# Optimization experiments

Measured on AMD Instinct MI355X. Metric: run time of the kernel, lower is better.

## Reference

```python
import jax, jax.numpy as jnp
import numpy as np

B, S, H, D = 2, 2048, 16, 64


def setup_inputs() -> dict:
    key0 = jax.random.key(0)
    kq, kk = jax.random.split(key0)
    query = jax.random.normal(kq, (B, S, H, D), dtype=jnp.float32)
    key = jax.random.normal(kk, (B, S, H, D), dtype=jnp.float32)
    # causal mask, broadcastable to [B, H, q, k]
    mask = jnp.tril(jnp.ones((S, S), dtype=bool))[None, None, :, :]
    mask = jnp.broadcast_to(mask, (B, 1, S, S))
    return {"query": query, "key": key, "mask": mask}


def reference(query, key, mask):
    dtype = query.dtype
    qk_features = query.shape[-1]
    q = query / jnp.sqrt(qk_features).astype(dtype)
    # [B, H, q, k]
    attn_weights = jnp.einsum('...qhd,...khd->...hqk', q, key)
    big_neg = jnp.finfo(dtype).min
    attn_weights = jnp.where(mask, attn_weights, big_neg)
    attn_weights = jax.nn.softmax(attn_weights).astype(dtype)
    return attn_weights
```

## Files before the change

### kernel.cpp

```cpp
#include <hip/hip_runtime.h>
#include <stdint.h>
#include <stddef.h>

#define B_ 2
#define H_ 16
#define S_ 2048
#define D_ 64

#define TQ 32
#define TK 256
#define NW 4
#define BLK (NW*64)
#define NQT (S_/TQ)
#define NBLK_F (B_*H_*NQT)
#define NBLK_S (32*36)
#define NBLK_W (32*8*4)

typedef __attribute__((ext_vector_type(8))) short bf16x8;
typedef __attribute__((ext_vector_type(4))) float f32x4;

__device__ __forceinline__ unsigned short f2bf(float f) {
  union { float f; uint32_t u; } v; v.f = f;
  uint32_t r = v.u + 0x7FFFu + ((v.u >> 16) & 1u);
  return (unsigned short)(r >> 16);
}

__device__ __forceinline__ void stage_k(const f32x4* kp, unsigned short* ldsK,
                                        int b, int h, int kc, int tid) {
#pragma unroll
  for (int i = 0; i < 8; ++i) {
    const int g  = i * BLK + tid;
    const int kl = g >> 3;
    const int gd = g & 7;
    const size_t gb = (((size_t)b * S_ + (kc * TK + kl)) * H_ + h) * (D_ / 4) + gd * 2;
    f32x4 v0 = kp[gb];
    f32x4 v1 = kp[gb + 1];
    bf16x8 bv;
    bv[0] = (short)f2bf(v0.x); bv[1] = (short)f2bf(v0.y);
    bv[2] = (short)f2bf(v0.z); bv[3] = (short)f2bf(v0.w);
    bv[4] = (short)f2bf(v1.x); bv[5] = (short)f2bf(v1.y);
    bv[6] = (short)f2bf(v1.z); bv[7] = (short)f2bf(v1.w);
    const int idx = (kl * D_ + gd * 8) ^ ((kl & 7) << 3);
    *reinterpret_cast<bf16x8*>(&ldsK[idx]) = bv;
  }
}

__device__ __forceinline__ void stage_q(const f32x4* qp, unsigned short (*ldsQ)[72],
                                        int b, int h, int qb, int tid) {
#pragma unroll
  for (int i = 0; i < 2; ++i) {
    const int g   = i * BLK + tid;
    const int row = g >> 4;
    const int d4  = g & 15;
    f32x4 v = qp[(((size_t)b * S_ + (qb + row)) * H_ + h) * (D_ / 4) + d4];
    unsigned short* dst = &ldsQ[row][d4 * 4];
    dst[0] = f2bf(v.x * 0.125f);
    dst[1] = f2bf(v.y * 0.125f);
    dst[2] = f2bf(v.z * 0.125f);
    dst[3] = f2bf(v.w * 0.125f);
  }
}

struct QPre { f32x4 a, b; };
__device__ __forceinline__ QPre qpre_load(const f32x4* qp, int b, int h, int qb, int tid) {
  QPre r;
  {
    const int g = tid;
    r.a = qp[(((size_t)b * S_ + (qb + (g >> 4))) * H_ + h) * (D_ / 4) + (g & 15)];
  }
  {
    const int g = BLK + tid;
    r.b = qp[(((size_t)b * S_ + (qb + (g >> 4))) * H_ + h) * (D_ / 4) + (g & 15)];
  }
  return r;
}
__device__ __forceinline__ void qpre_write(unsigned short (*ldsQ)[72], const QPre& p, int tid) {
#pragma unroll
  for (int i = 0; i < 2; ++i) {
    const int g   = i * BLK + tid;
    const int row = g >> 4;
    const int d4  = g & 15;
    const f32x4 v = i ? p.b : p.a;
    unsigned short* dst = &ldsQ[row][d4 * 4];
    dst[0] = f2bf(v.x * 0.125f);
    dst[1] = f2bf(v.y * 0.125f);
    dst[2] = f2bf(v.z * 0.125f);
    dst[3] = f2bf(v.w * 0.125f);
  }
}

__device__ __forceinline__ void load_qfr(const unsigned short (*ldsQ)[72],
                                         bf16x8 qfr[2][2], int colk, int rg) {
#pragma unroll
  for (int qf = 0; qf < 2; ++qf)
#pragma unroll
    for (int hh = 0; hh < 2; ++hh)
      qfr[qf][hh] = *reinterpret_cast<const bf16x8*>(&ldsQ[qf * 16 + colk][hh * 32 + rg * 8]);
}

__device__ __forceinline__ void mfma_tile(const unsigned short* ldsK,
                                          const bf16x8 qfr[2][2],
                                          f32x4 acc[4][2], int w, int colk, int rg) {
#pragma unroll
  for (int kf = 0; kf < 4; ++kf) {
    const int krow = w * 64 + kf * 16 + colk;
    const int i0 = (krow * D_ + rg * 8) ^ ((krow & 7) << 3);
    const int i1 = (krow * D_ + 32 + rg * 8) ^ ((krow & 7) << 3);
    bf16x8 a0 = *reinterpret_cast<const bf16x8*>(&ldsK[i0]);
    bf16x8 a1 = *reinterpret_cast<const bf16x8*>(&ldsK[i1]);
#pragma unroll
    for (int qf = 0; qf < 2; ++qf) {
      acc[kf][qf] = __builtin_amdgcn_mfma_f32_16x16x32_bf16(a0, qfr[qf][0], acc[kf][qf], 0, 0, 0);
      acc[kf][qf] = __builtin_amdgcn_mfma_f32_16x16x32_bf16(a1, qfr[qf][1], acc[kf][qf], 0, 0, 0);
    }
  }
}

__global__ __launch_bounds__(BLK, 4)
void attn_sums_v4(const float* __restrict__ Qg, const float* __restrict__ Kg,
                  float* __restrict__ wsPart) {
  __shared__ unsigned short ldsK[TK * D_];
  __shared__ unsigned short ldsQ[TQ][72];
  __shared__ float ldsSum[NW][2][16];

  const int tid  = threadIdx.x;
  const int lane = tid & 63;
  const int w    = tid >> 6;
  const int colk = lane & 15;
  const int rg   = lane >> 4;

  int bid = (int)blockIdx.x;
  bid = (bid & 7) * (NBLK_S / 8) + (bid >> 3);
  const int bh = bid / 36;
  int j = bid - bh * 36;
  int kc = 0, base = 0;
  while (j >= base + (8 - kc)) { base += 8 - kc; ++kc; }
  const int ci = j - base;
  const int qt0 = kc * 8 + ci * 8;
  const int b = bh >> 4, h = bh & (H_ - 1);

  const f32x4* qp = reinterpret_cast<const f32x4*>(Qg);
  const f32x4* kp = reinterpret_cast<const f32x4*>(Kg);

  stage_k(kp, ldsK, b, h, kc, tid);

  for (int i = 0; i < 8; ++i) {
    const int qt = qt0 + i;
    const int qb = qt * TQ;
    __syncthreads();
    stage_q(qp, ldsQ, b, h, qb, tid);
    __syncthreads();
    bf16x8 qfr[2][2];
    load_qfr(ldsQ, qfr, colk, rg);
    f32x4 acc[4][2];
#pragma unroll
    for (int kf = 0; kf < 4; ++kf)
#pragma unroll
      for (int qf = 0; qf < 2; ++qf) acc[kf][qf] = (f32x4)0.0f;
    mfma_tile(ldsK, qfr, acc, w, colk, rg);

    float rsum[2] = {0.f, 0.f};
#pragma unroll
    for (int kf = 0; kf < 4; ++kf)
#pragma unroll
      for (int qf = 0; qf < 2; ++qf)
#pragma unroll
        for (int r = 0; r < 4; ++r) {
          const int kk = kc * TK + w * 64 + kf * 16 + rg * 4 + r;
          const int qq = qb + qf * 16 + colk;
          rsum[qf] += (kk <= qq) ? __expf(acc[kf][qf][r]) : 0.f;
        }
#pragma unroll
    for (int qf = 0; qf < 2; ++qf) {
      float v = rsum[qf];
      v += __shfl_xor(v, 16);
      v += __shfl_xor(v, 32);
      rsum[qf] = v;
    }
    if (rg == 0) { ldsSum[w][0][colk] = rsum[0]; ldsSum[w][1][colk] = rsum[1]; }
    __syncthreads();
    if (tid < 32) {
      const int qf = tid >> 4, ck = tid & 15;
      const float s = ldsSum[0][qf][ck] + ldsSum[1][qf][ck] +
                      ldsSum[2][qf][ck] + ldsSum[3][qf][ck];
      wsPart[((size_t)bh * 8 + kc) * S_ + qb + tid] = s;
    }
  }
}

__global__ __launch_bounds__(BLK, 4)
void attn_store_v6(const float* __restrict__ Qg, const float* __restrict__ Kg,
                   const float* __restrict__ wsPart, float* __restrict__ Og) {
  __shared__ unsigned short ldsK[TK * D_];
  __shared__ unsigned short ldsQ[TQ][72];
  __shared__ float rinvL[512];

  const int tid  = threadIdx.x;
  const int lane = tid & 63;
  const int w    = tid >> 6;
  const int colk = lane & 15;
  const int rg   = lane >> 4;

  int bid = (int)blockIdx.x;
  bid = (bid & 7) * (NBLK_W / 8) + (bid >> 3);
  const int bh = bid >> 5;
  const int r5 = bid & 31;
  const int kc = r5 >> 2;
  const int qg = r5 & 3;
  const int b = bh >> 4, h = bh & (H_ - 1);
  const int kmin = kc * TK;
  const int row0 = qg * 512;

  if (kmin > row0 + 511) {
    f32x4 z = {0.f, 0.f, 0.f, 0.f};
#pragma unroll 4
    for (int it = 0; it < 128; ++it) {
      const int g = it * BLK + tid;
      const int row = row0 + (g >> 6);
      const int cg = g & 63;
      __builtin_nontemporal_store(z, reinterpret_cast<f32x4*>(
          Og + ((size_t)bh * S_ + row) * S_ + kmin + cg * 4));
    }
    return;
  }

  const f32x4* qp = reinterpret_cast<const f32x4*>(Qg);
  const f32x4* kp = reinterpret_cast<const f32x4*>(Kg);

  const int i0 = (kmin > row0) ? ((kmin - row0) >> 5) : 0;

  if (i0 > 0) {
    f32x4 z = {0.f, 0.f, 0.f, 0.f};
#pragma unroll 4
    for (int it = 0; it < 64; ++it) {
      const int g = it * BLK + tid;
      const int row = row0 + (g >> 6);
      const int cg = g & 63;
      __builtin_nontemporal_store(z, reinterpret_cast<f32x4*>(
          Og + ((size_t)bh * S_ + row) * S_ + kmin + cg * 4));
    }
  }

  stage_k(kp, ldsK, b, h, kc, tid);

  for (int lr = tid; lr < 512; lr += BLK) {
    const int q = row0 + lr;
    if (q >= kmin) {
      float s = 0.f;
      const int top = q >> 8;
      for (int c2 = 0; c2 <= top; ++c2)
        s += wsPart[((size_t)bh * 8 + c2) * S_ + q];
      rinvL[lr] = 1.0f / s;
    }
  }

  stage_q(qp, ldsQ, b, h, row0 + i0 * TQ, tid);
  __syncthreads();

  QPre pre;
  if (i0 + 1 < 16) pre = qpre_load(qp, b, h, row0 + (i0 + 1) * TQ, tid);

  for (int i = i0; i < 16; ++i) {
    const int qb = row0 + i * TQ;
    float* outT = Og + ((size_t)bh * S_ + qb) * S_ + kmin;

    bf16x8 qfr[2][2];
    load_qfr(ldsQ, qfr, colk, rg);
    asm volatile("s_waitcnt lgkmcnt(0)" ::: "memory");
    __builtin_amdgcn_sched_barrier(0);
    __builtin_amdgcn_s_barrier();

    if (i + 1 < 16) {
      qpre_write(ldsQ, pre, tid);
      if (i + 2 < 16) pre = qpre_load(qp, b, h, row0 + (i + 2) * TQ, tid);
      asm volatile("s_waitcnt lgkmcnt(0)" ::: "memory");
    }
    __builtin_amdgcn_s_barrier();

    f32x4 acc[4][2];
#pragma unroll
    for (int kf = 0; kf < 4; ++kf)
#pragma unroll
      for (int qf = 0; qf < 2; ++qf) acc[kf][qf] = (f32x4)0.0f;
    mfma_tile(ldsK, qfr, acc, w, colk, rg);

#pragma unroll
    for (int kf = 0; kf < 4; ++kf)
#pragma unroll
      for (int qf = 0; qf < 2; ++qf) {
        const int qq = qb + qf * 16 + colk;
        const float ri = rinvL[i * 32 + qf * 16 + colk];
        f32x4 o;
#pragma unroll
        for (int r = 0; r < 4; ++r) {
          const int kk = kmin + w * 64 + kf * 16 + rg * 4 + r;
          o[r] = (kk <= qq) ? __expf(acc[kf][qf][r]) * ri : 0.f;
        }
        __builtin_nontemporal_store(o, reinterpret_cast<f32x4*>(
            outT + (size_t)(qf * 16 + colk) * S_ + w * 64 + kf * 16 + rg * 4));
      }
  }
}

__global__ __launch_bounds__(BLK, 4)
void attn_weights_fused(const float* __restrict__ Qg, const float* __restrict__ Kg,
                        float* __restrict__ Og) {
  __shared__ unsigned short ldsK[TK * D_];
  __shared__ unsigned short ldsQ[TQ][72];
  __shared__ float ldsSum[NW][2][16];

  const int tid  = threadIdx.x;
  const int lane = tid & 63;
  const int w    = tid >> 6;
  const int colk = lane & 15;
  const int rg   = lane >> 4;

  int bid = (int)blockIdx.x;
  bid = (bid & 7) * (NBLK_F / 8) + (bid >> 3);
  const int qt = bid & (NQT - 1);
  const int bh = bid >> 6;
  const int h  = bh & (H_ - 1);
  const int b  = bh >> 4;
  const int qb = qt * TQ;
  const int tmax = qb >> 8;

  float* outp = Og + ((size_t)bh * S_ + qb) * S_;
  {
    const int row = tid >> 3;
    f32x4 z = {0.f, 0.f, 0.f, 0.f};
    float* rp = outp + (size_t)row * S_;
    for (int c = (tmax + 1) * (TK / 4) + (tid & 7); c < S_ / 4; c += 8)
      *reinterpret_cast<f32x4*>(rp + c * 4) = z;
  }
  const f32x4* qp = reinterpret_cast<const f32x4*>(Qg);
  const f32x4* kp = reinterpret_cast<const f32x4*>(Kg);
  stage_q(qp, ldsQ, b, h, qb, tid);
  __syncthreads();
  bf16x8 qfr[2][2];
  load_qfr(ldsQ, qfr, colk, rg);
  float rsum[2] = {0.f, 0.f};
  for (int t = 0; t <= tmax; ++t) {
    stage_k(kp, ldsK, b, h, t, tid);
    __syncthreads();
    f32x4 acc[4][2];
#pragma unroll
    for (int kf = 0; kf < 4; ++kf)
#pragma unroll
      for (int qf = 0; qf < 2; ++qf) acc[kf][qf] = (f32x4)0.0f;
    mfma_tile(ldsK, qfr, acc, w, colk, rg);
#pragma unroll
    for (int kf = 0; kf < 4; ++kf)
#pragma unroll
      for (int qf = 0; qf < 2; ++qf)
#pragma unroll
        for (int r = 0; r < 4; ++r) {
          const int kk = t * TK + w * 64 + kf * 16 + rg * 4 + r;
          const int qq = qb + qf * 16 + colk;
          rsum[qf] += (kk <= qq) ? __expf(acc[kf][qf][r]) : 0.f;
        }
    __syncthreads();
  }
#pragma unroll
  for (int qf = 0; qf < 2; ++qf) {
    float v = rsum[qf];
    v += __shfl_xor(v, 16);
    v += __shfl_xor(v, 32);
    rsum[qf] = v;
  }
  if (rg == 0) { ldsSum[w][0][colk] = rsum[0]; ldsSum[w][1][colk] = rsum[1]; }
  __syncthreads();
  float rinv[2];
#pragma unroll
  for (int qf = 0; qf < 2; ++qf)
    rinv[qf] = 1.0f / (ldsSum[0][qf][colk] + ldsSum[1][qf][colk] +
                       ldsSum[2][qf][colk] + ldsSum[3][qf][colk]);
  for (int t = 0; t <= tmax; ++t) {
    stage_k(kp, ldsK, b, h, t, tid);
    __syncthreads();
    f32x4 acc[4][2];
#pragma unroll
    for (int kf = 0; kf < 4; ++kf)
#pragma unroll
      for (int qf = 0; qf < 2; ++qf) acc[kf][qf] = (f32x4)0.0f;
    mfma_tile(ldsK, qfr, acc, w, colk, rg);
#pragma unroll
    for (int kf = 0; kf < 4; ++kf)
#pragma unroll
      for (int qf = 0; qf < 2; ++qf) {
        f32x4 o;
#pragma unroll
        for (int r = 0; r < 4; ++r) {
          const int kk = t * TK + w * 64 + kf * 16 + rg * 4 + r;
          const int qq = qb + qf * 16 + colk;
          o[r] = (kk <= qq) ? __expf(acc[kf][qf][r]) * rinv[qf] : 0.f;
        }
        *reinterpret_cast<f32x4*>(outp + (size_t)(qf * 16 + colk) * S_ +
                                  t * TK + w * 64 + kf * 16 + rg * 4) = o;
      }
    __syncthreads();
  }
}

extern "C" void kernel_launch(void* const* d_in, const int* in_sizes, int n_in,
                              void* d_out, int out_size, void* d_ws, size_t ws_size,
                              hipStream_t stream) {
  const float* Qg = (const float*)d_in[0];
  const float* Kg = (const float*)d_in[1];
  float* Og = (float*)d_out;
  const size_t need = (size_t)32 * 8 * S_ * sizeof(float);
  if (ws_size >= need) {
    float* wsPart = (float*)d_ws;
    attn_sums_v4 <<<dim3(NBLK_S), dim3(BLK), 0, stream>>>(Qg, Kg, wsPart);
    attn_store_v6<<<dim3(NBLK_W), dim3(BLK), 0, stream>>>(Qg, Kg, wsPart, Og);
  } else {
    attn_weights_fused<<<dim3(NBLK_F), dim3(BLK), 0, stream>>>(Qg, Kg, Og);
  }
}
```

Before: 154.4 us.

## Move zero-fill of upper-triangle tiles into the sums kernel to overlap compute

The first kernel now also owns the zero-fill blocks. These are interleaved with the row-sum blocks so that memory-bound zero stores overlap compute-bound sums, and the store kernel launches only the 640 tiles that need exp and normalisation. This removes the earlier idle early-exit blocks and evens out the store kernel's workload. In exchange, the grid-index remapping of the first kernel grows more complex, and the old bid swizzle is dropped there.

Measured after the change: 175.9 us. 14.0% more time.

```diff
diff --git a/kernel.cpp b/kernel.cpp
--- a/kernel.cpp
+++ b/kernel.cpp
@@ -13,8 +13,10 @@
 #define BLK (NW*64)
 #define NQT (S_/TQ)
 #define NBLK_F (B_*H_*NQT)
-#define NBLK_S (32*36)
-#define NBLK_W (32*8*4)
+#define NS_SUM 1152
+#define NS_ZERO 512
+#define NBLK_P (NS_SUM+NS_ZERO)
+#define NBLK_W 640
 
 typedef __attribute__((ext_vector_type(8))) short bf16x8;
 typedef __attribute__((ext_vector_type(4))) float f32x4;
@@ -117,8 +119,8 @@
 }
 
 __global__ __launch_bounds__(BLK, 4)
-void attn_sums_v4(const float* __restrict__ Qg, const float* __restrict__ Kg,
-                  float* __restrict__ wsPart) {
+void attn_pre(const float* __restrict__ Qg, const float* __restrict__ Kg,
+              float* __restrict__ wsPart, float* __restrict__ Og) {
   __shared__ unsigned short ldsK[TK * D_];
   __shared__ unsigned short ldsQ[TQ][72];
   __shared__ float ldsSum[NW][2][16];
@@ -129,10 +131,44 @@
   const int colk = lane & 15;
   const int rg   = lane >> 4;
 
-  int bid = (int)blockIdx.x;
-  bid = (bid & 7) * (NBLK_S / 8) + (bid >> 3);
-  const int bh = bid / 36;
-  int j = bid - bh * 36;
+  const int raw = (int)blockIdx.x;
+
+  if (raw < 2 * NS_ZERO && (raw & 1)) {
+    const int z  = raw >> 1;
+    const int bh = z >> 4;
+    const int p  = z & 15;
+    f32x4 zf = {0.f, 0.f, 0.f, 0.f};
+    if (p < 12) {
+      const int qg = (p < 6) ? 0 : (p < 10) ? 1 : 2;
+      const int kc = (qg == 0) ? 2 + p : (qg == 1) ? p - 2 : p - 4;
+      const int row0 = qg * 512, kmin = kc * TK;
+#pragma unroll 4
+      for (int it = 0; it < 128; ++it) {
+        const int g = it * BLK + tid;
+        const int row = row0 + (g >> 6);
+        const int cg = g & 63;
+        __builtin_nontemporal_store(zf, reinterpret_cast<f32x4*>(
+            Og + ((size_t)bh * S_ + row) * S_ + kmin + cg * 4));
+      }
+    } else {
+      const int pr = p - 12;
+      const int qg = pr, kc = 2 * pr + 1;
+      const int row0 = qg * 512, kmin = kc * TK;
+#pragma unroll 4
+      for (int it = 0; it < 64; ++it) {
+        const int g = it * BLK + tid;
+        const int row = row0 + (g >> 6);
+        const int cg = g & 63;
+        __builtin_nontemporal_store(zf, reinterpret_cast<f32x4*>(
+            Og + ((size_t)bh * S_ + row) * S_ + kmin + cg * 4));
+      }
+    }
+    return;
+  }
+
+  const int si = (raw < 2 * NS_ZERO) ? (raw >> 1) : (raw - NS_ZERO);
+  const int bh = si / 36;
+  int j = si % 36;
   int kc = 0, base = 0;
   while (j >= base + (8 - kc)) { base += 8 - kc; ++kc; }
   const int ci = j - base;
@@ -145,8 +181,7 @@
   stage_k(kp, ldsK, b, h, kc, tid);
 
   for (int i = 0; i < 8; ++i) {
-    const int qt = qt0 + i;
-    const int qb = qt * TQ;
+    const int qb = (qt0 + i) * TQ;
     __syncthreads();
     stage_q(qp, ldsQ, b, h, qb, tid);
     __syncthreads();
@@ -189,7 +224,7 @@
 }
 
 __global__ __launch_bounds__(BLK, 4)
-void attn_store_v6(const float* __restrict__ Qg, const float* __restrict__ Kg,
+void attn_store_v7(const float* __restrict__ Qg, const float* __restrict__ Kg,
                    const float* __restrict__ wsPart, float* __restrict__ Og) {
   __shared__ unsigned short ldsK[TK * D_];
   __shared__ unsigned short ldsQ[TQ][72];
@@ -203,43 +238,18 @@
 
   int bid = (int)blockIdx.x;
   bid = (bid & 7) * (NBLK_W / 8) + (bid >> 3);
-  const int bh = bid >> 5;
-  const int r5 = bid & 31;
-  const int kc = r5 >> 2;
-  const int qg = r5 & 3;
+  const int bh = bid / 20;
+  const int r  = bid % 20;
+  const int qg = (r < 2) ? 0 : (r < 6) ? 1 : (r < 12) ? 2 : 3;
+  const int kc = (qg == 0) ? r : (qg == 1) ? r - 2 : (qg == 2) ? r - 6 : r - 12;
   const int b = bh >> 4, h = bh & (H_ - 1);
   const int kmin = kc * TK;
   const int row0 = qg * 512;
 
-  if (kmin > row0 + 511) {
-    f32x4 z = {0.f, 0.f, 0.f, 0.f};
-#pragma unroll 4
-    for (int it = 0; it < 128; ++it) {
-      const int g = it * BLK + tid;
-      const int row = row0 + (g >> 6);
-      const int cg = g & 63;
-      __builtin_nontemporal_store(z, reinterpret_cast<f32x4*>(
-          Og + ((size_t)bh * S_ + row) * S_ + kmin + cg * 4));
-    }
-    return;
-  }
-
   const f32x4* qp = reinterpret_cast<const f32x4*>(Qg);
   const f32x4* kp = reinterpret_cast<const f32x4*>(Kg);
 
   const int i0 = (kmin > row0) ? ((kmin - row0) >> 5) : 0;
-
-  if (i0 > 0) {
-    f32x4 z = {0.f, 0.f, 0.f, 0.f};
-#pragma unroll 4
-    for (int it = 0; it < 64; ++it) {
-      const int g = it * BLK + tid;
-      const int row = row0 + (g >> 6);
-      const int cg = g & 63;
-      __builtin_nontemporal_store(z, reinterpret_cast<f32x4*>(
-          Og + ((size_t)bh * S_ + row) * S_ + kmin + cg * 4));
-    }
-  }
 
   stage_k(kp, ldsK, b, h, kc, tid);
 
@@ -292,9 +302,9 @@
         const float ri = rinvL[i * 32 + qf * 16 + colk];
         f32x4 o;
 #pragma unroll
-        for (int r = 0; r < 4; ++r) {
-          const int kk = kmin + w * 64 + kf * 16 + rg * 4 + r;
-          o[r] = (kk <= qq) ? __expf(acc[kf][qf][r]) * ri : 0.f;
+        for (int r2 = 0; r2 < 4; ++r2) {
+          const int kk = kmin + w * 64 + kf * 16 + rg * 4 + r2;
+          o[r2] = (kk <= qq) ? __expf(acc[kf][qf][r2]) * ri : 0.f;
         }
         __builtin_nontemporal_store(o, reinterpret_cast<f32x4*>(
             outT + (size_t)(qf * 16 + colk) * S_ + w * 64 + kf * 16 + rg * 4));
@@ -410,8 +420,8 @@
   const size_t need = (size_t)32 * 8 * S_ * sizeof(float);
   if (ws_size >= need) {
     float* wsPart = (float*)d_ws;
-    attn_sums_v4 <<<dim3(NBLK_S), dim3(BLK), 0, stream>>>(Qg, Kg, wsPart);
-    attn_store_v6<<<dim3(NBLK_W), dim3(BLK), 0, stream>>>(Qg, Kg, wsPart, Og);
+    attn_pre     <<<dim3(NBLK_P), dim3(BLK), 0, stream>>>(Qg, Kg, wsPart, Og);
+    attn_store_v7<<<dim3(NBLK_W), dim3(BLK), 0, stream>>>(Qg, Kg, wsPart, Og);
   } else {
     attn_weights_fused<<<dim3(NBLK_F), dim3(BLK), 0, stream>>>(Qg, Kg, Og);
   }
```

## Pipeline Q staging with register prefetch and skip fully-masked K fragments in sums kernel

Applied to the files above, without the earlier changes.

Restructures the row-sum kernel so the next Q tile is prefetched into registers and written to LDS while the current tile is processed, cutting the barriers per iteration from three to two. The workspace write for each tile is deferred to the next iteration. MFMA work for K fragments lying entirely above the causal diagonal is skipped. The cost is hand-placed waitcnt and barrier ordering, which is fragile, and QPre/qpre_load/qpre_write helpers that must already exist in the unseen code.

Result: slower. 157.7 us (+2.2%).

```diff
diff --git a/kernel.cpp b/kernel.cpp
--- a/kernel.cpp
+++ b/kernel.cpp
@@ -117,7 +117,7 @@
 }
 
 __global__ __launch_bounds__(BLK, 4)
-void attn_sums_v4(const float* __restrict__ Qg, const float* __restrict__ Kg,
+void attn_sums_v6(const float* __restrict__ Qg, const float* __restrict__ Kg,
                   float* __restrict__ wsPart) {
   __shared__ unsigned short ldsK[TK * D_];
   __shared__ unsigned short ldsQ[TQ][72];
@@ -143,33 +143,57 @@
   const f32x4* kp = reinterpret_cast<const f32x4*>(Kg);
 
   stage_k(kp, ldsK, b, h, kc, tid);
+  stage_q(qp, ldsQ, b, h, qt0 * TQ, tid);
+  __syncthreads();
+
+  QPre pre = qpre_load(qp, b, h, (qt0 + 1) * TQ, tid);
 
   for (int i = 0; i < 8; ++i) {
-    const int qt = qt0 + i;
-    const int qb = qt * TQ;
-    __syncthreads();
-    stage_q(qp, ldsQ, b, h, qb, tid);
-    __syncthreads();
+    const int qb = (qt0 + i) * TQ;
+
     bf16x8 qfr[2][2];
     load_qfr(ldsQ, qfr, colk, rg);
-    f32x4 acc[4][2];
-#pragma unroll
-    for (int kf = 0; kf < 4; ++kf)
-#pragma unroll
-      for (int qf = 0; qf < 2; ++qf) acc[kf][qf] = (f32x4)0.0f;
-    mfma_tile(ldsK, qfr, acc, w, colk, rg);
+    asm volatile("s_waitcnt lgkmcnt(0)" ::: "memory");
+    __builtin_amdgcn_sched_barrier(0);
+    __builtin_amdgcn_s_barrier();
+
+    if (i > 0 && tid < 32) {
+      const int qf = tid >> 4, ck = tid & 15;
+      const float s = ldsSum[0][qf][ck] + ldsSum[1][qf][ck] +
+                      ldsSum[2][qf][ck] + ldsSum[3][qf][ck];
+      wsPart[((size_t)bh * 8 + kc) * S_ + (qb - TQ) + tid] = s;
+    }
+
+    if (i + 1 < 8) {
+      qpre_write(ldsQ, pre, tid);
+      if (i + 2 < 8) pre = qpre_load(qp, b, h, (qt0 + i + 2) * TQ, tid);
+      asm volatile("s_waitcnt lgkmcnt(0)" ::: "memory");
+    }
+    __builtin_amdgcn_s_barrier();
 
     float rsum[2] = {0.f, 0.f};
 #pragma unroll
-    for (int kf = 0; kf < 4; ++kf)
-#pragma unroll
-      for (int qf = 0; qf < 2; ++qf)
-#pragma unroll
-        for (int r = 0; r < 4; ++r) {
-          const int kk = kc * TK + w * 64 + kf * 16 + rg * 4 + r;
+    for (int kf = 0; kf < 4; ++kf) {
+      if (kc * TK + w * 64 + kf * 16 <= qb + 31) {
+        const int krow = w * 64 + kf * 16 + colk;
+        const int a0i = (krow * D_ + rg * 8) ^ ((krow & 7) << 3);
+        const int a1i = (krow * D_ + 32 + rg * 8) ^ ((krow & 7) << 3);
+        bf16x8 a0 = *reinterpret_cast<const bf16x8*>(&ldsK[a0i]);
+        bf16x8 a1 = *reinterpret_cast<const bf16x8*>(&ldsK[a1i]);
+#pragma unroll
+        for (int qf = 0; qf < 2; ++qf) {
+          f32x4 acc = (f32x4)0.0f;
+          acc = __builtin_amdgcn_mfma_f32_16x16x32_bf16(a0, qfr[qf][0], acc, 0, 0, 0);
+          acc = __builtin_amdgcn_mfma_f32_16x16x32_bf16(a1, qfr[qf][1], acc, 0, 0, 0);
           const int qq = qb + qf * 16 + colk;
-          rsum[qf] += (kk <= qq) ? __expf(acc[kf][qf][r]) : 0.f;
+#pragma unroll
+          for (int r = 0; r < 4; ++r) {
+            const int kk = kc * TK + w * 64 + kf * 16 + rg * 4 + r;
+            rsum[qf] += (kk <= qq) ? __expf(acc[r]) : 0.f;
+          }
         }
+      }
+    }
 #pragma unroll
     for (int qf = 0; qf < 2; ++qf) {
       float v = rsum[qf];
@@ -178,13 +202,14 @@
       rsum[qf] = v;
     }
     if (rg == 0) { ldsSum[w][0][colk] = rsum[0]; ldsSum[w][1][colk] = rsum[1]; }
-    __syncthreads();
-    if (tid < 32) {
-      const int qf = tid >> 4, ck = tid & 15;
-      const float s = ldsSum[0][qf][ck] + ldsSum[1][qf][ck] +
-                      ldsSum[2][qf][ck] + ldsSum[3][qf][ck];
-      wsPart[((size_t)bh * 8 + kc) * S_ + qb + tid] = s;
-    }
+  }
+
+  __syncthreads();
+  if (tid < 32) {
+    const int qf = tid >> 4, ck = tid & 15;
+    const float s = ldsSum[0][qf][ck] + ldsSum[1][qf][ck] +
+                    ldsSum[2][qf][ck] + ldsSum[3][qf][ck];
+    wsPart[((size_t)bh * 8 + kc) * S_ + (qt0 + 7) * TQ + tid] = s;
   }
 }
 
@@ -410,7 +435,7 @@
   const size_t need = (size_t)32 * 8 * S_ * sizeof(float);
   if (ws_size >= need) {
     float* wsPart = (float*)d_ws;
-    attn_sums_v4 <<<dim3(NBLK_S), dim3(BLK), 0, stream>>>(Qg, Kg, wsPart);
+    attn_sums_v6 <<<dim3(NBLK_S), dim3(BLK), 0, stream>>>(Qg, Kg, wsPart);
     attn_store_v6<<<dim3(NBLK_W), dim3(BLK), 0, stream>>>(Qg, Kg, wsPart, Og);
   } else {
     attn_weights_fused<<<dim3(NBLK_F), dim3(BLK), 0, stream>>>(Qg, Kg, Og);
```
